# Performance work log

Measured on AMD Instinct MI355X. Metric: run time of the kernel, lower is better.

The kernel has to match this reference:

```python
import jax, jax.numpy as jnp
import numpy as np

L, B, K = 512, 1024, 64
START_IDX, STOP_IDX = 62, 63
NEG_INF = -10000.0


def setup_inputs() -> dict:
    key = jax.random.key(0)
    k1, k2, k3, k4 = jax.random.split(key, 4)
    emit_scores = jax.random.normal(k1, (L, B, K), dtype=jnp.float32)
    labels = jax.random.randint(k2, (L, B), 0, 60)  # avoid START/STOP in gold labels
    lengths = jax.random.randint(k3, (B,), L // 4, L + 1)
    masks = (jnp.arange(L)[:, None] < lengths[None, :]).astype(jnp.float32)
    transitions = jax.random.normal(k4, (K, K), dtype=jnp.float32)
    return {"emit_scores": emit_scores, "transitions": transitions,
            "labels": labels, "masks": masks}


def _partition(emit_scores, transitions, masks):
    Bc = masks.shape[1]
    Kc = transitions.shape[0]
    init = jnp.full((Bc, Kc), NEG_INF, dtype=emit_scores.dtype).at[:, START_IDX].set(0.0)

    def step(prev, inp):
        emit_t, mask_t = inp  # (B,K), (B,)
        # new[b,k] = logsumexp_j(prev[b,j] + trans[k,j]) + emit_t[b,k]
        new = jax.nn.logsumexp(prev[:, None, :] + transitions[None, :, :], axis=2) + emit_t
        new = jnp.where(mask_t[:, None] > 0, new, prev)  # carry state on padded steps
        return new, None

    final, _ = jax.lax.scan(step, init, (emit_scores, masks))
    return jax.nn.logsumexp(final + transitions[STOP_IDX][None, :], axis=1)  # (B,)


def _sent_score(emit_scores, transitions, labels, masks):
    Lc, Bc = masks.shape
    lab = jnp.concatenate(
        [jnp.full((1, Bc), START_IDX, dtype=labels.dtype), labels], axis=0)  # (L+1,B)
    trans_sc = transitions[lab[1:], lab[:-1]]  # (L,B): score(prev -> cur)
    emit_sc = jnp.take_along_axis(emit_scores, lab[1:][:, :, None], axis=2)[..., 0]  # (L,B)
    score = jnp.sum((trans_sc + emit_sc) * masks, axis=0)  # (B,)
    lengths = jnp.sum(masks, axis=0).astype(jnp.int32)
    last_label = lab[lengths, jnp.arange(Bc)]  # last real label per sequence
    return score + transitions[STOP_IDX, last_label]


def reference(emit_scores, transitions, labels, masks):
    # CRF negative log-likelihood per sequence: log Z - gold path score
    partition = _partition(emit_scores, transitions, masks)
    gold = _sent_score(emit_scores, transitions, labels, masks)
    return partition - gold  # (B,)
```

## Files before the change

kernel.cpp:

```cpp
#include <hip/hip_runtime.h>

namespace {
constexpr int L_ = 512;
constexpr int B_ = 1024;
constexpr int K_ = 64;
constexpr int START_I = 62;
constexpr int STOP_I = 63;
}

__device__ __forceinline__ float bcast0(float x) {
    return __int_as_float(__builtin_amdgcn_readfirstlane(__float_as_int(x)));
}

#define MAC4(k, Ea, Eb, Ec, Ed)                                             \
    {                                                                       \
        float pa = __int_as_float(__builtin_amdgcn_readlane(pi, (k)));      \
        float pb = __int_as_float(__builtin_amdgcn_readlane(pi, (k) + 1));  \
        float pc = __int_as_float(__builtin_amdgcn_readlane(pi, (k) + 2));  \
        float pd = __int_as_float(__builtin_amdgcn_readlane(pi, (k) + 3));  \
        a0 = fmaf(pa, Ea, a0);                                              \
        a1 = fmaf(pb, Eb, a1);                                              \
        a2 = fmaf(pc, Ec, a2);                                              \
        a3 = fmaf(pd, Ed, a3);                                              \
    }

#define CRF_STEP(EREG, TNEXT, RECEN)                                        \
    do {                                                                    \
        float ee = exp2f(EREG * 1.4426950408889634f);                       \
        {                                                                   \
            int tp = (TNEXT) < len ? (TNEXT) : (len - 1);                   \
            EREG = eb[(long)tp * (B_ * K_)];                                \
        }                                                                   \
        int pi = __float_as_int(p);                                         \
        float a0 = 0.f, a1 = 0.f, a2 = 0.f, a3 = 0.f;                       \
        MAC4(0,  E0,  E1,  E2,  E3)   MAC4(4,  E4,  E5,  E6,  E7)           \
        MAC4(8,  E8,  E9,  E10, E11)  MAC4(12, E12, E13, E14, E15)          \
        MAC4(16, E16, E17, E18, E19)  MAC4(20, E20, E21, E22, E23)          \
        MAC4(24, E24, E25, E26, E27)  MAC4(28, E28, E29, E30, E31)          \
        MAC4(32, E32, E33, E34, E35)  MAC4(36, E36, E37, E38, E39)          \
        MAC4(40, E40, E41, E42, E43)  MAC4(44, E44, E45, E46, E47)          \
        MAC4(48, E48, E49, E50, E51)  MAC4(52, E52, E53, E54, E55)          \
        MAC4(56, E56, E57, E58, E59)  MAC4(60, E60, E61, E62, E63)          \
        float pn = ((a0 + a1) + (a2 + a3)) * ee;                            \
        if (RECEN) {                                                        \
            float p0 = bcast0(pn);                                          \
            int kk = (int)(__float_as_uint(p0) >> 23) - 127;                \
            pn *= __uint_as_float((unsigned)(127 - kk) << 23);              \
            base2 += (float)kk;                                             \
        }                                                                   \
        p = pn;                                                             \
    } while (0)

__global__ __launch_bounds__(64)
__attribute__((amdgpu_waves_per_eu(1, 1)))
void crf_kernel(
    const float* __restrict__ emit,
    const float* __restrict__ trans,
    const int* __restrict__ labels,
    const float* __restrict__ masks,
    float* __restrict__ out)
{
    const int lane = threadIdx.x & 63;
    const int b = blockIdx.x;
    constexpr float LOG2E = 1.4426950408889634f;
    constexpr float LN2 = 0.6931471805599453f;

    const float4* t4 = reinterpret_cast<const float4*>(trans + lane * K_);
#define MKE(q, A, Bn, C, D)                                                 \
    float4 tv##q = t4[q];                                                   \
    float A  = exp2f(tv##q.x * LOG2E);                                      \
    float Bn = exp2f(tv##q.y * LOG2E);                                      \
    float C  = exp2f(tv##q.z * LOG2E);                                      \
    float D  = exp2f(tv##q.w * LOG2E);                                      \
    asm("" : "+v"(A), "+v"(Bn), "+v"(C), "+v"(D));
    MKE(0,  E0,  E1,  E2,  E3)   MKE(1,  E4,  E5,  E6,  E7)
    MKE(2,  E8,  E9,  E10, E11)  MKE(3,  E12, E13, E14, E15)
    MKE(4,  E16, E17, E18, E19)  MKE(5,  E20, E21, E22, E23)
    MKE(6,  E24, E25, E26, E27)  MKE(7,  E28, E29, E30, E31)
    MKE(8,  E32, E33, E34, E35)  MKE(9,  E36, E37, E38, E39)
    MKE(10, E40, E41, E42, E43)  MKE(11, E44, E45, E46, E47)
    MKE(12, E48, E49, E50, E51)  MKE(13, E52, E53, E54, E55)
    MKE(14, E56, E57, E58, E59)  MKE(15, E60, E61, E62, E63)
#undef MKE

    int len = 0;
    #pragma unroll
    for (int c = 0; c < L_ / 64; ++c)
        len += (int)masks[(c * 64 + lane) * B_ + b];
    #pragma unroll
    for (int off = 32; off >= 1; off >>= 1)
        len += __shfl_xor(len, off);

    float p = (lane == START_I) ? 1.0f : 0.0f;
    float base2 = 0.0f;
    const float* eb = emit + b * K_ + lane;

    float e0 = eb[0L * (B_ * K_)];
    float e1 = eb[1L * (B_ * K_)];
    float e2 = eb[2L * (B_ * K_)];
    float e3 = eb[3L * (B_ * K_)];

    int t = 0;
    for (; t + 4 <= len; t += 4) {
        CRF_STEP(e0, t + 4, 0);
        CRF_STEP(e1, t + 5, 0);
        CRF_STEP(e2, t + 6, 0);
        CRF_STEP(e3, t + 7, 1);
    }
    if (t < len) { CRF_STEP(e0, len - 1, 1); ++t; }
    if (t < len) { CRF_STEP(e1, len - 1, 1); ++t; }
    if (t < len) { CRF_STEP(e2, len - 1, 1); ++t; }

    float v = fmaf(__log2f(p) + base2, LN2, trans[STOP_I * K_ + lane]);
    float M = v;
    #pragma unroll
    for (int off = 32; off >= 1; off >>= 1)
        M = fmaxf(M, __shfl_xor(M, off));
    float pe = exp2f((v - M) * LOG2E);
    #pragma unroll
    for (int off = 32; off >= 1; off >>= 1)
        pe += __shfl_xor(pe, off);
    float part = fmaf(__log2f(pe), LN2, M);

    float g = 0.0f;
    #pragma unroll
    for (int c = 0; c < L_ / 64; ++c) {
        int tt = c * 64 + lane;
        if (tt < len) {
            int lt = labels[tt * B_ + b];
            int lp;
            if (tt == 0) lp = START_I;
            else lp = labels[(tt - 1) * B_ + b];
            g += trans[lt * K_ + lp] + emit[((long)tt * B_ + b) * K_ + lt];
        }
    }
    #pragma unroll
    for (int off = 32; off >= 1; off >>= 1)
        g += __shfl_xor(g, off);
    int lastl = labels[(len - 1) * B_ + b];
    g += trans[STOP_I * K_ + lastl];

    if (lane == 0) out[b] = part - g;
}

extern "C" void kernel_launch(void* const* d_in, const int* in_sizes, int n_in,
                              void* d_out, int out_size, void* d_ws, size_t ws_size,
                              hipStream_t stream) {
    const float* emit = (const float*)d_in[0];
    const float* trans = (const float*)d_in[1];
    const int* labels = (const int*)d_in[2];
    const float* masks = (const float*)d_in[3];
    float* out = (float*)d_out;
    crf_kernel<<<B_, 64, 0, stream>>>(emit, trans, labels, masks, out);
}
```

Before: 130.5 us.

## Replace readlane broadcasts with DPP row rotations and bpermute in CRF matvec

Each recurrence step's 64x64 mat-vec previously used 64 scalar readlane broadcasts. It now uses three ds_bpermute calls to gather the other 16-lane row blocks, plus DPP row_ror rotations inside each row, so every lane reads a different source. The exp(transitions) registers are re-indexed per lane to match the rotated order, with a runtime check on the rotation direction. This is meant to move work off the scalar/readlane path onto the VALU with DPP modifiers, at the cost of LDS-latency bpermutes on the serial dependency chain.

```diff
diff --git a/kernel.cpp b/kernel.cpp
--- a/kernel.cpp
+++ b/kernel.cpp
@@ -12,17 +12,27 @@
     return __int_as_float(__builtin_amdgcn_readfirstlane(__float_as_int(x)));
 }
 
-#define MAC4(k, Ea, Eb, Ec, Ed)                                             \
-    {                                                                       \
-        float pa = __int_as_float(__builtin_amdgcn_readlane(pi, (k)));      \
-        float pb = __int_as_float(__builtin_amdgcn_readlane(pi, (k) + 1));  \
-        float pc = __int_as_float(__builtin_amdgcn_readlane(pi, (k) + 2));  \
-        float pd = __int_as_float(__builtin_amdgcn_readlane(pi, (k) + 3));  \
-        a0 = fmaf(pa, Ea, a0);                                              \
-        a1 = fmaf(pb, Eb, a1);                                              \
-        a2 = fmaf(pc, Ec, a2);                                              \
-        a3 = fmaf(pd, Ed, a3);                                              \
-    }
+#define DPPF(x, ctl)                                                        \
+    __int_as_float(__builtin_amdgcn_update_dpp(                             \
+        0, __float_as_int(x), (ctl), 0xF, 0xF, false))
+
+#define FROW(acc, c, Ea)                                                    \
+    acc = fmaf((c),           Ea##_0,  acc);                                \
+    acc = fmaf(DPPF(c,0x121), Ea##_1,  acc);                                \
+    acc = fmaf(DPPF(c,0x122), Ea##_2,  acc);                                \
+    acc = fmaf(DPPF(c,0x123), Ea##_3,  acc);                                \
+    acc = fmaf(DPPF(c,0x124), Ea##_4,  acc);                                \
+    acc = fmaf(DPPF(c,0x125), Ea##_5,  acc);                                \
+    acc = fmaf(DPPF(c,0x126), Ea##_6,  acc);                                \
+    acc = fmaf(DPPF(c,0x127), Ea##_7,  acc);                                \
+    acc = fmaf(DPPF(c,0x128), Ea##_8,  acc);                                \
+    acc = fmaf(DPPF(c,0x129), Ea##_9,  acc);                                \
+    acc = fmaf(DPPF(c,0x12A), Ea##_10, acc);                                \
+    acc = fmaf(DPPF(c,0x12B), Ea##_11, acc);                                \
+    acc = fmaf(DPPF(c,0x12C), Ea##_12, acc);                                \
+    acc = fmaf(DPPF(c,0x12D), Ea##_13, acc);                                \
+    acc = fmaf(DPPF(c,0x12E), Ea##_14, acc);                                \
+    acc = fmaf(DPPF(c,0x12F), Ea##_15, acc);
 
 #define CRF_STEP(EREG, TNEXT, RECEN)                                        \
     do {                                                                    \
@@ -31,16 +41,15 @@
             int tp = (TNEXT) < len ? (TNEXT) : (len - 1);                   \
             EREG = eb[(long)tp * (B_ * K_)];                                \
         }                                                                   \
-        int pi = __float_as_int(p);                                         \
+        int pi_ = __float_as_int(p);                                        \
+        float c1 = __int_as_float(__builtin_amdgcn_ds_bpermute(A16, pi_));  \
+        float c2 = __int_as_float(__builtin_amdgcn_ds_bpermute(A32, pi_));  \
+        float c3 = __int_as_float(__builtin_amdgcn_ds_bpermute(A48, pi_));  \
         float a0 = 0.f, a1 = 0.f, a2 = 0.f, a3 = 0.f;                       \
-        MAC4(0,  E0,  E1,  E2,  E3)   MAC4(4,  E4,  E5,  E6,  E7)           \
-        MAC4(8,  E8,  E9,  E10, E11)  MAC4(12, E12, E13, E14, E15)          \
-        MAC4(16, E16, E17, E18, E19)  MAC4(20, E20, E21, E22, E23)          \
-        MAC4(24, E24, E25, E26, E27)  MAC4(28, E28, E29, E30, E31)          \
-        MAC4(32, E32, E33, E34, E35)  MAC4(36, E36, E37, E38, E39)          \
-        MAC4(40, E40, E41, E42, E43)  MAC4(44, E44, E45, E46, E47)          \
-        MAC4(48, E48, E49, E50, E51)  MAC4(52, E52, E53, E54, E55)          \
-        MAC4(56, E56, E57, E58, E59)  MAC4(60, E60, E61, E62, E63)          \
+        FROW(a0, p,  Er0)                                                   \
+        FROW(a1, c1, Er1)                                                   \
+        FROW(a2, c2, Er2)                                                   \
+        FROW(a3, c3, Er3)                                                   \
         float pn = ((a0 + a1) + (a2 + a3)) * ee;                            \
         if (RECEN) {                                                        \
             float p0 = bcast0(pn);                                          \
@@ -65,23 +74,27 @@
     constexpr float LOG2E = 1.4426950408889634f;
     constexpr float LN2 = 0.6931471805599453f;
 
-    const float4* t4 = reinterpret_cast<const float4*>(trans + lane * K_);
-#define MKE(q, A, Bn, C, D)                                                 \
-    float4 tv##q = t4[q];                                                   \
-    float A  = exp2f(tv##q.x * LOG2E);                                      \
-    float Bn = exp2f(tv##q.y * LOG2E);                                      \
-    float C  = exp2f(tv##q.z * LOG2E);                                      \
-    float D  = exp2f(tv##q.w * LOG2E);                                      \
-    asm("" : "+v"(A), "+v"(Bn), "+v"(C), "+v"(D));
-    MKE(0,  E0,  E1,  E2,  E3)   MKE(1,  E4,  E5,  E6,  E7)
-    MKE(2,  E8,  E9,  E10, E11)  MKE(3,  E12, E13, E14, E15)
-    MKE(4,  E16, E17, E18, E19)  MKE(5,  E20, E21, E22, E23)
-    MKE(6,  E24, E25, E26, E27)  MKE(7,  E28, E29, E30, E31)
-    MKE(8,  E32, E33, E34, E35)  MKE(9,  E36, E37, E38, E39)
-    MKE(10, E40, E41, E42, E43)  MKE(11, E44, E45, E46, E47)
-    MKE(12, E48, E49, E50, E51)  MKE(13, E52, E53, E54, E55)
-    MKE(14, E56, E57, E58, E59)  MKE(15, E60, E61, E62, E63)
-#undef MKE
+    int w = __builtin_amdgcn_update_dpp(0, lane, 0x121, 0xF, 0xF, false);
+    int sgn = (__builtin_amdgcn_readfirstlane(w) == 15) ? -1 : 1;
+
+    const int A16 = ((lane + 16) & 63) * 4;
+    const int A32 = ((lane + 32) & 63) * 4;
+    const int A48 = ((lane + 48) & 63) * 4;
+
+#define MKER(a, r)                                                          \
+    float Er##a##_##r = exp2f(                                              \
+        trans[lane * K_ +                                                   \
+              (((lane & 48) + ((lane + sgn * (r)) & 15) + 16 * (a)) & 63)]  \
+        * LOG2E);                                                           \
+    asm("" : "+v"(Er##a##_##r));
+#define MKERA(a)                                                            \
+    MKER(a, 0)  MKER(a, 1)  MKER(a, 2)  MKER(a, 3)                          \
+    MKER(a, 4)  MKER(a, 5)  MKER(a, 6)  MKER(a, 7)                          \
+    MKER(a, 8)  MKER(a, 9)  MKER(a, 10) MKER(a, 11)                         \
+    MKER(a, 12) MKER(a, 13) MKER(a, 14) MKER(a, 15)
+    MKERA(0) MKERA(1) MKERA(2) MKERA(3)
+#undef MKERA
+#undef MKER
 
     int len = 0;
     #pragma unroll
```

After: 204.1 us. 56.4% more time.

## Split CRF forward recursion across two waves per sequence via LDS exchange

Applied to the files above, without the earlier changes.

Each sequence now uses two 64-lane waves, and each wave computes the partial sum over half of the 64 previous states, so each wave holds only 32 exp-transition registers. The two partial sums are exchanged through double-buffered shared memory with a __syncthreads every step. This halves the serial readlane/FMA chain per step but adds a block barrier and LDS round trip on every one of up to 512 sequential steps. The 1024 sequences are spread over twice as many waves, which may or may not raise CU utilisation.

```diff
diff --git a/kernel.cpp b/kernel.cpp
--- a/kernel.cpp
+++ b/kernel.cpp
@@ -12,36 +12,37 @@
     return __int_as_float(__builtin_amdgcn_readfirstlane(__float_as_int(x)));
 }
 
-#define MAC4(k, Ea, Eb, Ec, Ed)                                             \
-    {                                                                       \
-        float pa = __int_as_float(__builtin_amdgcn_readlane(pi, (k)));      \
-        float pb = __int_as_float(__builtin_amdgcn_readlane(pi, (k) + 1));  \
-        float pc = __int_as_float(__builtin_amdgcn_readlane(pi, (k) + 2));  \
-        float pd = __int_as_float(__builtin_amdgcn_readlane(pi, (k) + 3));  \
-        a0 = fmaf(pa, Ea, a0);                                              \
-        a1 = fmaf(pb, Eb, a1);                                              \
-        a2 = fmaf(pc, Ec, a2);                                              \
-        a3 = fmaf(pd, Ed, a3);                                              \
-    }
+#define RLJ(k) __int_as_float(__builtin_amdgcn_readlane(pi_, jb + (k)))
 
-#define CRF_STEP(EREG, TNEXT, RECEN)                                        \
+#define CRF_STEP(EREG, TNEXT, PAR, RECEN)                                   \
     do {                                                                    \
         float ee = exp2f(EREG * 1.4426950408889634f);                       \
         {                                                                   \
             int tp = (TNEXT) < len ? (TNEXT) : (len - 1);                   \
             EREG = eb[(long)tp * (B_ * K_)];                                \
         }                                                                   \
-        int pi = __float_as_int(p);                                         \
+        int pi_ = __float_as_int(p);                                        \
         float a0 = 0.f, a1 = 0.f, a2 = 0.f, a3 = 0.f;                       \
-        MAC4(0,  E0,  E1,  E2,  E3)   MAC4(4,  E4,  E5,  E6,  E7)           \
-        MAC4(8,  E8,  E9,  E10, E11)  MAC4(12, E12, E13, E14, E15)          \
-        MAC4(16, E16, E17, E18, E19)  MAC4(20, E20, E21, E22, E23)          \
-        MAC4(24, E24, E25, E26, E27)  MAC4(28, E28, E29, E30, E31)          \
-        MAC4(32, E32, E33, E34, E35)  MAC4(36, E36, E37, E38, E39)          \
-        MAC4(40, E40, E41, E42, E43)  MAC4(44, E44, E45, E46, E47)          \
-        MAC4(48, E48, E49, E50, E51)  MAC4(52, E52, E53, E54, E55)          \
-        MAC4(56, E56, E57, E58, E59)  MAC4(60, E60, E61, E62, E63)          \
-        float pn = ((a0 + a1) + (a2 + a3)) * ee;                            \
+        a0 = fmaf(RLJ(0),  E0,  a0); a1 = fmaf(RLJ(8),  E8,  a1);           \
+        a2 = fmaf(RLJ(16), E16, a2); a3 = fmaf(RLJ(24), E24, a3);           \
+        a0 = fmaf(RLJ(1),  E1,  a0); a1 = fmaf(RLJ(9),  E9,  a1);           \
+        a2 = fmaf(RLJ(17), E17, a2); a3 = fmaf(RLJ(25), E25, a3);           \
+        a0 = fmaf(RLJ(2),  E2,  a0); a1 = fmaf(RLJ(10), E10, a1);           \
+        a2 = fmaf(RLJ(18), E18, a2); a3 = fmaf(RLJ(26), E26, a3);           \
+        a0 = fmaf(RLJ(3),  E3,  a0); a1 = fmaf(RLJ(11), E11, a1);           \
+        a2 = fmaf(RLJ(19), E19, a2); a3 = fmaf(RLJ(27), E27, a3);           \
+        a0 = fmaf(RLJ(4),  E4,  a0); a1 = fmaf(RLJ(12), E12, a1);           \
+        a2 = fmaf(RLJ(20), E20, a2); a3 = fmaf(RLJ(28), E28, a3);           \
+        a0 = fmaf(RLJ(5),  E5,  a0); a1 = fmaf(RLJ(13), E13, a1);           \
+        a2 = fmaf(RLJ(21), E21, a2); a3 = fmaf(RLJ(29), E29, a3);           \
+        a0 = fmaf(RLJ(6),  E6,  a0); a1 = fmaf(RLJ(14), E14, a1);           \
+        a2 = fmaf(RLJ(22), E22, a2); a3 = fmaf(RLJ(30), E30, a3);           \
+        a0 = fmaf(RLJ(7),  E7,  a0); a1 = fmaf(RLJ(15), E15, a1);           \
+        a2 = fmaf(RLJ(23), E23, a2); a3 = fmaf(RLJ(31), E31, a3);           \
+        float mine = (a0 + a1) + (a2 + a3);                                 \
+        xbuf[PAR][wid][lane] = mine;                                        \
+        __syncthreads();                                                    \
+        float pn = (mine + xbuf[PAR][wid ^ 1][lane]) * ee;                  \
         if (RECEN) {                                                        \
             float p0 = bcast0(pn);                                          \
             int kk = (int)(__float_as_uint(p0) >> 23) - 127;                \
@@ -51,8 +52,7 @@
         p = pn;                                                             \
     } while (0)
 
-__global__ __launch_bounds__(64)
-__attribute__((amdgpu_waves_per_eu(1, 1)))
+__global__ __launch_bounds__(128, 2)
 void crf_kernel(
     const float* __restrict__ emit,
     const float* __restrict__ trans,
@@ -60,27 +60,25 @@
     const float* __restrict__ masks,
     float* __restrict__ out)
 {
+    __shared__ float xbuf[2][2][64];
     const int lane = threadIdx.x & 63;
+    const int wid = threadIdx.x >> 6;
+    const int jb = wid << 5;
     const int b = blockIdx.x;
     constexpr float LOG2E = 1.4426950408889634f;
     constexpr float LN2 = 0.6931471805599453f;
 
-    const float4* t4 = reinterpret_cast<const float4*>(trans + lane * K_);
+    const float* tr = trans + lane * K_ + jb;
 #define MKE(q, A, Bn, C, D)                                                 \
-    float4 tv##q = t4[q];                                                   \
-    float A  = exp2f(tv##q.x * LOG2E);                                      \
-    float Bn = exp2f(tv##q.y * LOG2E);                                      \
-    float C  = exp2f(tv##q.z * LOG2E);                                      \
-    float D  = exp2f(tv##q.w * LOG2E);                                      \
+    float A  = exp2f(tr[4 * (q) + 0] * LOG2E);                              \
+    float Bn = exp2f(tr[4 * (q) + 1] * LOG2E);                              \
+    float C  = exp2f(tr[4 * (q) + 2] * LOG2E);                              \
+    float D  = exp2f(tr[4 * (q) + 3] * LOG2E);                              \
     asm("" : "+v"(A), "+v"(Bn), "+v"(C), "+v"(D));
-    MKE(0,  E0,  E1,  E2,  E3)   MKE(1,  E4,  E5,  E6,  E7)
-    MKE(2,  E8,  E9,  E10, E11)  MKE(3,  E12, E13, E14, E15)
-    MKE(4,  E16, E17, E18, E19)  MKE(5,  E20, E21, E22, E23)
-    MKE(6,  E24, E25, E26, E27)  MKE(7,  E28, E29, E30, E31)
-    MKE(8,  E32, E33, E34, E35)  MKE(9,  E36, E37, E38, E39)
-    MKE(10, E40, E41, E42, E43)  MKE(11, E44, E45, E46, E47)
-    MKE(12, E48, E49, E50, E51)  MKE(13, E52, E53, E54, E55)
-    MKE(14, E56, E57, E58, E59)  MKE(15, E60, E61, E62, E63)
+    MKE(0, E0,  E1,  E2,  E3)   MKE(1, E4,  E5,  E6,  E7)
+    MKE(2, E8,  E9,  E10, E11)  MKE(3, E12, E13, E14, E15)
+    MKE(4, E16, E17, E18, E19)  MKE(5, E20, E21, E22, E23)
+    MKE(6, E24, E25, E26, E27)  MKE(7, E28, E29, E30, E31)
 #undef MKE
 
     int len = 0;
@@ -102,14 +100,14 @@
 
     int t = 0;
     for (; t + 4 <= len; t += 4) {
-        CRF_STEP(e0, t + 4, 0);
-        CRF_STEP(e1, t + 5, 0);
-        CRF_STEP(e2, t + 6, 0);
-        CRF_STEP(e3, t + 7, 1);
+        CRF_STEP(e0, t + 4, 0, 0);
+        CRF_STEP(e1, t + 5, 1, 0);
+        CRF_STEP(e2, t + 6, 0, 0);
+        CRF_STEP(e3, t + 7, 1, 1);
     }
-    if (t < len) { CRF_STEP(e0, len - 1, 1); ++t; }
-    if (t < len) { CRF_STEP(e1, len - 1, 1); ++t; }
-    if (t < len) { CRF_STEP(e2, len - 1, 1); ++t; }
+    if (t < len) { CRF_STEP(e0, len - 1, 0, 1); ++t; }
+    if (t < len) { CRF_STEP(e1, len - 1, 1, 1); ++t; }
+    if (t < len) { CRF_STEP(e2, len - 1, 0, 1); ++t; }
 
     float v = fmaf(__log2f(p) + base2, LN2, trans[STOP_I * K_ + lane]);
     float M = v;
@@ -122,25 +120,25 @@
         pe += __shfl_xor(pe, off);
     float part = fmaf(__log2f(pe), LN2, M);
 
-    float g = 0.0f;
-    #pragma unroll
-    for (int c = 0; c < L_ / 64; ++c) {
-        int tt = c * 64 + lane;
-        if (tt < len) {
-            int lt = labels[tt * B_ + b];
-            int lp;
-            if (tt == 0) lp = START_I;
-            else lp = labels[(tt - 1) * B_ + b];
-            g += trans[lt * K_ + lp] + emit[((long)tt * B_ + b) * K_ + lt];
+    if (wid == 0) {
+        float g = 0.0f;
+        #pragma unroll
+        for (int c = 0; c < L_ / 64; ++c) {
+            int tt = c * 64 + lane;
+            if (tt < len) {
+                int lt = labels[tt * B_ + b];
+                int lp = (tt == 0) ? START_I : labels[(tt - 1) * B_ + b];
+                g += trans[lt * K_ + lp] + emit[((long)tt * B_ + b) * K_ + lt];
+            }
         }
+        #pragma unroll
+        for (int off = 32; off >= 1; off >>= 1)
+            g += __shfl_xor(g, off);
+        int lastl = labels[(len - 1) * B_ + b];
+        g += trans[STOP_I * K_ + lastl];
+
+        if (lane == 0) out[b] = part - g;
     }
-    #pragma unroll
-    for (int off = 32; off >= 1; off >>= 1)
-        g += __shfl_xor(g, off);
-    int lastl = labels[(len - 1) * B_ + b];
-    g += trans[STOP_I * K_ + lastl];
-
-    if (lane == 0) out[b] = part - g;
 }
 
 extern "C" void kernel_launch(void* const* d_in, const int* in_sizes, int n_in,
@@ -151,5 +149,5 @@
     const int* labels = (const int*)d_in[2];
     const float* masks = (const float*)d_in[3];
     float* out = (float*)d_out;
-    crf_kernel<<<B_, 64, 0, stream>>>(emit, trans, labels, masks, out);
+    crf_kernel<<<B_, 128, 0, stream>>>(emit, trans, labels, masks, out);
 }
```

Measured after the change: 240.1 us. 1.84x slower.

## Use packed fp16 dot2 for CRF forward recurrence with per-step rescaling

Applied to the files above, without the earlier changes.

Converts the exponentiated transition matrix and the per-step probability vector to packed fp16 pairs and uses v_dot2 instructions. This halves the readlane broadcasts and the multiply-add count in the serial 64x64 recurrence. To keep the values inside fp16 range, it renormalises every step instead of every fourth, peels the first four steps, and makes len wave-uniform. The risk is precision loss, since fp16 products with exp(transitions) spanning several orders of magnitude may hurt accuracy.

```diff
diff --git a/kernel.cpp b/kernel.cpp
--- a/kernel.cpp
+++ b/kernel.cpp
@@ -8,45 +8,54 @@
 constexpr int STOP_I = 63;
 }
 
-__device__ __forceinline__ float bcast0(float x) {
-    return __int_as_float(__builtin_amdgcn_readfirstlane(__float_as_int(x)));
-}
+typedef _Float16 h2 __attribute__((ext_vector_type(2)));
+typedef unsigned int u32;
 
-#define MAC4(k, Ea, Eb, Ec, Ed)                                             \
+#define LOG2E 1.4426950408889634f
+#define LN2 0.6931471805599453f
+
+#define CVTPK2(x, y) \
+    __builtin_bit_cast(h2, __builtin_amdgcn_cvt_pkrtz((x), (y)))
+
+#if __has_builtin(__builtin_amdgcn_fdot2)
+#define FDOT2(a, b, c) __builtin_amdgcn_fdot2((a), (b), (c), false)
+#else
+#define FDOT2(a, b, c) \
+    fmaf((float)(a).x, (float)(b).x, fmaf((float)(a).y, (float)(b).y, (c)))
+#endif
+
+#define DT(k, ACC)                                                          \
     {                                                                       \
-        float pa = __int_as_float(__builtin_amdgcn_readlane(pi, (k)));      \
-        float pb = __int_as_float(__builtin_amdgcn_readlane(pi, (k) + 1));  \
-        float pc = __int_as_float(__builtin_amdgcn_readlane(pi, (k) + 2));  \
-        float pd = __int_as_float(__builtin_amdgcn_readlane(pi, (k) + 3));  \
-        a0 = fmaf(pa, Ea, a0);                                              \
-        a1 = fmaf(pb, Eb, a1);                                              \
-        a2 = fmaf(pc, Ec, a2);                                              \
-        a3 = fmaf(pd, Ed, a3);                                              \
+        int s_ = __builtin_amdgcn_readlane(pki, 2 * (k));                   \
+        ACC = FDOT2(__builtin_bit_cast(h2, s_), E##k, ACC);                 \
     }
 
 #define CRF_STEP(EREG, TNEXT, RECEN)                                        \
     do {                                                                    \
-        float ee = exp2f(EREG * 1.4426950408889634f);                       \
+        float ee = exp2f(EREG * LOG2E);                                     \
         {                                                                   \
             int tp = (TNEXT) < len ? (TNEXT) : (len - 1);                   \
             EREG = eb[(long)tp * (B_ * K_)];                                \
         }                                                                   \
-        int pi = __float_as_int(p);                                         \
+        int pi_ = __float_as_int(p);                                        \
+        int nbi = __builtin_amdgcn_update_dpp(0, pi_, 0xB1, 0xF, 0xF, false);\
+        h2 pk2 = CVTPK2(p, __int_as_float(nbi));                            \
+        int pki = __builtin_bit_cast(int, pk2);                             \
         float a0 = 0.f, a1 = 0.f, a2 = 0.f, a3 = 0.f;                       \
-        MAC4(0,  E0,  E1,  E2,  E3)   MAC4(4,  E4,  E5,  E6,  E7)           \
-        MAC4(8,  E8,  E9,  E10, E11)  MAC4(12, E12, E13, E14, E15)          \
-        MAC4(16, E16, E17, E18, E19)  MAC4(20, E20, E21, E22, E23)          \
-        MAC4(24, E24, E25, E26, E27)  MAC4(28, E28, E29, E30, E31)          \
-        MAC4(32, E32, E33, E34, E35)  MAC4(36, E36, E37, E38, E39)          \
-        MAC4(40, E40, E41, E42, E43)  MAC4(44, E44, E45, E46, E47)          \
-        MAC4(48, E48, E49, E50, E51)  MAC4(52, E52, E53, E54, E55)          \
-        MAC4(56, E56, E57, E58, E59)  MAC4(60, E60, E61, E62, E63)          \
+        DT(0, a0)  DT(1, a1)  DT(2, a2)  DT(3, a3)                          \
+        DT(4, a0)  DT(5, a1)  DT(6, a2)  DT(7, a3)                          \
+        DT(8, a0)  DT(9, a1)  DT(10, a2) DT(11, a3)                         \
+        DT(12, a0) DT(13, a1) DT(14, a2) DT(15, a3)                         \
+        DT(16, a0) DT(17, a1) DT(18, a2) DT(19, a3)                         \
+        DT(20, a0) DT(21, a1) DT(22, a2) DT(23, a3)                         \
+        DT(24, a0) DT(25, a1) DT(26, a2) DT(27, a3)                         \
+        DT(28, a0) DT(29, a1) DT(30, a2) DT(31, a3)                         \
         float pn = ((a0 + a1) + (a2 + a3)) * ee;                            \
         if (RECEN) {                                                        \
-            float p0 = bcast0(pn);                                          \
-            int kk = (int)(__float_as_uint(p0) >> 23) - 127;                \
-            pn *= __uint_as_float((unsigned)(127 - kk) << 23);              \
-            base2 += (float)kk;                                             \
+            int p0i = __builtin_amdgcn_readfirstlane(__float_as_int(pn));   \
+            int kk = ((p0i >> 23) & 0xFF) - 127;                            \
+            pn *= __uint_as_float((u32)(127 - kk) << 23);                   \
+            base2k += kk;                                                   \
         }                                                                   \
         p = pn;                                                             \
     } while (0)
@@ -62,25 +71,17 @@
 {
     const int lane = threadIdx.x & 63;
     const int b = blockIdx.x;
-    constexpr float LOG2E = 1.4426950408889634f;
-    constexpr float LN2 = 0.6931471805599453f;
 
     const float4* t4 = reinterpret_cast<const float4*>(trans + lane * K_);
-#define MKE(q, A, Bn, C, D)                                                 \
+#define MKE(q, A, Bn)                                                       \
     float4 tv##q = t4[q];                                                   \
-    float A  = exp2f(tv##q.x * LOG2E);                                      \
-    float Bn = exp2f(tv##q.y * LOG2E);                                      \
-    float C  = exp2f(tv##q.z * LOG2E);                                      \
-    float D  = exp2f(tv##q.w * LOG2E);                                      \
-    asm("" : "+v"(A), "+v"(Bn), "+v"(C), "+v"(D));
-    MKE(0,  E0,  E1,  E2,  E3)   MKE(1,  E4,  E5,  E6,  E7)
-    MKE(2,  E8,  E9,  E10, E11)  MKE(3,  E12, E13, E14, E15)
-    MKE(4,  E16, E17, E18, E19)  MKE(5,  E20, E21, E22, E23)
-    MKE(6,  E24, E25, E26, E27)  MKE(7,  E28, E29, E30, E31)
-    MKE(8,  E32, E33, E34, E35)  MKE(9,  E36, E37, E38, E39)
-    MKE(10, E40, E41, E42, E43)  MKE(11, E44, E45, E46, E47)
-    MKE(12, E48, E49, E50, E51)  MKE(13, E52, E53, E54, E55)
-    MKE(14, E56, E57, E58, E59)  MKE(15, E60, E61, E62, E63)
+    h2 A  = CVTPK2(exp2f(tv##q.x * LOG2E), exp2f(tv##q.y * LOG2E));         \
+    h2 Bn = CVTPK2(exp2f(tv##q.z * LOG2E), exp2f(tv##q.w * LOG2E));         \
+    asm("" : "+v"(A), "+v"(Bn));
+    MKE(0, E0, E1)   MKE(1, E2, E3)   MKE(2, E4, E5)   MKE(3, E6, E7)
+    MKE(4, E8, E9)   MKE(5, E10, E11) MKE(6, E12, E13) MKE(7, E14, E15)
+    MKE(8, E16, E17) MKE(9, E18, E19) MKE(10, E20, E21) MKE(11, E22, E23)
+    MKE(12, E24, E25) MKE(13, E26, E27) MKE(14, E28, E29) MKE(15, E30, E31)
 #undef MKE
 
     int len = 0;
@@ -90,9 +91,10 @@
     #pragma unroll
     for (int off = 32; off >= 1; off >>= 1)
         len += __shfl_xor(len, off);
+    len = __builtin_amdgcn_readfirstlane(len);
 
     float p = (lane == START_I) ? 1.0f : 0.0f;
-    float base2 = 0.0f;
+    int base2k = 0;
     const float* eb = emit + b * K_ + lane;
 
     float e0 = eb[0L * (B_ * K_)];
@@ -100,17 +102,22 @@
     float e2 = eb[2L * (B_ * K_)];
     float e3 = eb[3L * (B_ * K_)];
 
-    int t = 0;
+    CRF_STEP(e0, 4, 0);
+    CRF_STEP(e1, 5, 1);
+    CRF_STEP(e2, 6, 1);
+    CRF_STEP(e3, 7, 1);
+    int t = 4;
     for (; t + 4 <= len; t += 4) {
-        CRF_STEP(e0, t + 4, 0);
-        CRF_STEP(e1, t + 5, 0);
-        CRF_STEP(e2, t + 6, 0);
+        CRF_STEP(e0, t + 4, 1);
+        CRF_STEP(e1, t + 5, 1);
+        CRF_STEP(e2, t + 6, 1);
         CRF_STEP(e3, t + 7, 1);
     }
     if (t < len) { CRF_STEP(e0, len - 1, 1); ++t; }
     if (t < len) { CRF_STEP(e1, len - 1, 1); ++t; }
     if (t < len) { CRF_STEP(e2, len - 1, 1); ++t; }
 
+    float base2 = (float)base2k;
     float v = fmaf(__log2f(p) + base2, LN2, trans[STOP_I * K_ + lane]);
     float M = v;
     #pragma unroll
@@ -128,9 +135,7 @@
         int tt = c * 64 + lane;
         if (tt < len) {
             int lt = labels[tt * B_ + b];
-            int lp;
-            if (tt == 0) lp = START_I;
-            else lp = labels[(tt - 1) * B_ + b];
+            int lp = (tt == 0) ? START_I : labels[(tt - 1) * B_ + b];
             g += trans[lt * K_ + lp] + emit[((long)tt * B_ + b) * K_ + lt];
         }
     }
```

After: 193.9 us. 1.49x slower.
